# Kernel optimization log

Measured on AMD Instinct MI355X. Metric: run time of the kernel, lower is better.

## Reference

```python
import jax, jax.numpy as jnp
import numpy as np

TOKENS, D_IN, D_OUT, RANK = 32768, 1024, 1024, 16
SCALE1 = 8.0 / RANK   # alpha=8, rank=16
SCALE2 = 16.0 / RANK  # alpha=16, rank=16


def setup_inputs() -> dict:
    key = jax.random.key(0)
    ks = jax.random.split(key, 7)
    inv = 1.0 / np.sqrt(D_IN)
    return {
        "x": jax.random.normal(ks[0], (TOKENS, D_IN), jnp.float32),
        "W": jax.random.normal(ks[1], (D_OUT, D_IN), jnp.float32) * inv,
        "b": jax.random.normal(ks[2], (D_OUT,), jnp.float32) * 0.01,
        "A1": jax.random.normal(ks[3], (RANK, D_IN), jnp.float32) * inv,
        "B1": jax.random.normal(ks[4], (D_OUT, RANK), jnp.float32) * 0.01,
        "A2": jax.random.normal(ks[5], (RANK, D_IN), jnp.float32) * inv,
        "B2": jax.random.normal(ks[6], (D_OUT, RANK), jnp.float32) * 0.01,
    }


def reference(x, W, b, A1, B1, A2, B2):
    # base linear: [T, D_in] @ [D_in, D_out] + b
    out = jnp.einsum("ti,oi->to", x, W) + b
    # LoRA adapter 1: scale * (x @ A1^T) @ B1^T   (dropout=Identity in eval)
    out = out + SCALE1 * jnp.einsum("tr,or->to", jnp.einsum("ti,ri->tr", x, A1), B1)
    # LoRA adapter 2
    out = out + SCALE2 * jnp.einsum("tr,or->to", jnp.einsum("ti,ri->tr", x, A2), B2)
    return out
```

## Files before the change

### kernel.cpp

```cpp
#include <hip/hip_runtime.h>

#define TOKENS 32768
#define DIN 1024
#define DOUT 1024
#define RANK 16
#define SCALE1 0.5f
#define SCALE2 1.0f

#define BM 128
#define BN 128
#define BK 32

typedef __bf16 bf16x8 __attribute__((ext_vector_type(8)));
typedef float f32x4 __attribute__((ext_vector_type(4)));

__device__ __forceinline__ void load_lds16(const void* gptr, void* lptr) {
    __builtin_amdgcn_global_load_lds(
        (__attribute__((address_space(1))) void*)gptr,
        (__attribute__((address_space(3))) void*)lptr, 16, 0, 0);
}

__global__ void weff_kernel(const float* __restrict__ W, const float* __restrict__ A1,
                            const float* __restrict__ B1, const float* __restrict__ A2,
                            const float* __restrict__ B2, __bf16* __restrict__ Weff) {
    int idx = blockIdx.x * blockDim.x + threadIdx.x;
    int o = idx >> 10;
    int i = idx & 1023;
    float s1 = 0.f, s2 = 0.f;
#pragma unroll
    for (int r = 0; r < RANK; ++r) {
        s1 += B1[o * RANK + r] * A1[r * DIN + i];
        s2 += B2[o * RANK + r] * A2[r * DIN + i];
    }
    Weff[idx] = (__bf16)(W[idx] + SCALE1 * s1 + SCALE2 * s2);
}

__global__ void cvt_x_kernel(const float* __restrict__ x, __bf16* __restrict__ xb) {
    int i = (blockIdx.x * blockDim.x + threadIdx.x) * 8;
    float4 a = *(const float4*)(x + i);
    float4 b = *(const float4*)(x + i + 4);
    bf16x8 v;
    v[0] = (__bf16)a.x; v[1] = (__bf16)a.y; v[2] = (__bf16)a.z; v[3] = (__bf16)a.w;
    v[4] = (__bf16)b.x; v[5] = (__bf16)b.y; v[6] = (__bf16)b.z; v[7] = (__bf16)b.w;
    *(bf16x8*)(xb + i) = v;
}

__global__ __launch_bounds__(256) void gemm_bt_kernel(
    const __bf16* __restrict__ A,
    const __bf16* __restrict__ Bw,
    const float* __restrict__ bias, float* __restrict__ C) {
    __shared__ __bf16 lsA[BM * BK];
    __shared__ __bf16 lsB[BN * BK];

    const int tid = threadIdx.x;
    const int wave = tid >> 6;
    const int lane = tid & 63;
    const int m0 = blockIdx.y * BM;
    const int n0 = blockIdx.x * BN;
    const int wm = wave >> 1;
    const int wn = wave & 1;

    const int lrow = lane >> 2;
    const int lcol = ((lane & 3) ^ ((lane >> 3) & 3)) * 8;

    const __bf16* gA = A + (size_t)(m0 + wave * 32 + lrow) * DIN + lcol;
    const __bf16* gB = Bw + (size_t)(n0 + wave * 32 + lrow) * DIN + lcol;
    __bf16* lA0 = &lsA[(wave * 32) * BK];
    __bf16* lA1 = &lsA[(wave * 32 + 16) * BK];
    __bf16* lB0 = &lsB[(wave * 32) * BK];
    __bf16* lB1 = &lsB[(wave * 32 + 16) * BK];

    f32x4 acc[4][4];
#pragma unroll
    for (int i = 0; i < 4; ++i)
#pragma unroll
        for (int j = 0; j < 4; ++j) acc[i][j] = f32x4{0.f, 0.f, 0.f, 0.f};

    const int fr = lane & 15;
    const int fsw = (((lane >> 4) ^ ((lane >> 1) & 3))) * 8;

    for (int k0 = 0; k0 < DIN; k0 += BK) {
        load_lds16(gA + k0, lA0);
        load_lds16(gA + k0 + 16 * DIN, lA1);
        load_lds16(gB + k0, lB0);
        load_lds16(gB + k0 + 16 * DIN, lB1);
        __syncthreads();

        bf16x8 af[4], bfv[4];
#pragma unroll
        for (int t = 0; t < 4; ++t) {
            af[t] = *(const bf16x8*)&lsA[(wm * 64 + t * 16 + fr) * BK + fsw];
            bfv[t] = *(const bf16x8*)&lsB[(wn * 64 + t * 16 + fr) * BK + fsw];
        }
#pragma unroll
        for (int mt = 0; mt < 4; ++mt)
#pragma unroll
            for (int nt = 0; nt < 4; ++nt)
                acc[mt][nt] = __builtin_amdgcn_mfma_f32_16x16x32_bf16(
                    af[mt], bfv[nt], acc[mt][nt], 0, 0, 0);
        __syncthreads();
    }

    const int rbase = (lane >> 4) * 4;
#pragma unroll
    for (int nt = 0; nt < 4; ++nt) {
        const int n = n0 + wn * 64 + nt * 16 + fr;
        const float bv = bias[n];
#pragma unroll
        for (int mt = 0; mt < 4; ++mt) {
            const int m = m0 + wm * 64 + mt * 16 + rbase;
            float* cp = C + (size_t)m * DOUT + n;
#pragma unroll
            for (int r = 0; r < 4; ++r) cp[(size_t)r * DOUT] = acc[mt][nt][r] + bv;
        }
    }
}

extern "C" void kernel_launch(void* const* d_in, const int* in_sizes, int n_in,
                              void* d_out, int out_size, void* d_ws, size_t ws_size,
                              hipStream_t stream) {
    const float* x  = (const float*)d_in[0];
    const float* W  = (const float*)d_in[1];
    const float* b  = (const float*)d_in[2];
    const float* A1 = (const float*)d_in[3];
    const float* B1 = (const float*)d_in[4];
    const float* A2 = (const float*)d_in[5];
    const float* B2 = (const float*)d_in[6];
    float* out = (float*)d_out;

    __bf16* xb   = (__bf16*)d_ws;
    __bf16* Weff = (__bf16*)((char*)d_ws + (size_t)TOKENS * DIN * sizeof(__bf16));

    cvt_x_kernel<<<TOKENS * DIN / (256 * 8), 256, 0, stream>>>(x, xb);
    weff_kernel<<<DOUT * DIN / 256, 256, 0, stream>>>(W, A1, B1, A2, B2, Weff);
    gemm_bt_kernel<<<dim3(DOUT / BN, TOKENS / BM), 256, 0, stream>>>(xb, Weff, b, out);
}
```

Measured before the change: 347.7 us.

## Double-buffer LDS tiles in GEMM to overlap global loads with MFMA

The GEMM kernel now keeps two LDS buffers for the A and B tiles. It prefetches the next K-tile with direct global-to-LDS loads while computing on the current one, which cuts the barriers per iteration from two to one. The aim is to hide global load latency behind the MFMA work. In exchange, LDS use per block doubles. The overlap may also be lost if the compiler inserts a conservative wait on the outstanding LDS-DMA loads before the fragment reads.

```diff
diff --git a/kernel.cpp b/kernel.cpp
--- a/kernel.cpp
+++ b/kernel.cpp
@@ -49,8 +49,8 @@
     const __bf16* __restrict__ A,
     const __bf16* __restrict__ Bw,
     const float* __restrict__ bias, float* __restrict__ C) {
-    __shared__ __bf16 lsA[BM * BK];
-    __shared__ __bf16 lsB[BN * BK];
+    __shared__ alignas(16) __bf16 lsA[2][BM * BK];
+    __shared__ alignas(16) __bf16 lsB[2][BN * BK];
 
     const int tid = threadIdx.x;
     const int wave = tid >> 6;
@@ -65,10 +65,8 @@
 
     const __bf16* gA = A + (size_t)(m0 + wave * 32 + lrow) * DIN + lcol;
     const __bf16* gB = Bw + (size_t)(n0 + wave * 32 + lrow) * DIN + lcol;
-    __bf16* lA0 = &lsA[(wave * 32) * BK];
-    __bf16* lA1 = &lsA[(wave * 32 + 16) * BK];
-    __bf16* lB0 = &lsB[(wave * 32) * BK];
-    __bf16* lB1 = &lsB[(wave * 32 + 16) * BK];
+    const int so0 = (wave * 32) * BK;
+    const int so1 = (wave * 32 + 16) * BK;
 
     f32x4 acc[4][4];
 #pragma unroll
@@ -77,20 +75,30 @@
         for (int j = 0; j < 4; ++j) acc[i][j] = f32x4{0.f, 0.f, 0.f, 0.f};
 
     const int fr = lane & 15;
-    const int fsw = (((lane >> 4) ^ ((lane >> 1) & 3))) * 8;
+    const int fsw = ((lane >> 4) ^ ((lane >> 1) & 3)) * 8;
 
+    load_lds16(gA, &lsA[0][so0]);
+    load_lds16(gA + 16 * DIN, &lsA[0][so1]);
+    load_lds16(gB, &lsB[0][so0]);
+    load_lds16(gB + 16 * DIN, &lsB[0][so1]);
+
+    int cur = 0;
     for (int k0 = 0; k0 < DIN; k0 += BK) {
-        load_lds16(gA + k0, lA0);
-        load_lds16(gA + k0 + 16 * DIN, lA1);
-        load_lds16(gB + k0, lB0);
-        load_lds16(gB + k0 + 16 * DIN, lB1);
         __syncthreads();
+
+        if (k0 + BK < DIN) {
+            const int kn = k0 + BK;
+            load_lds16(gA + kn, &lsA[cur ^ 1][so0]);
+            load_lds16(gA + kn + 16 * DIN, &lsA[cur ^ 1][so1]);
+            load_lds16(gB + kn, &lsB[cur ^ 1][so0]);
+            load_lds16(gB + kn + 16 * DIN, &lsB[cur ^ 1][so1]);
+        }
 
         bf16x8 af[4], bfv[4];
 #pragma unroll
         for (int t = 0; t < 4; ++t) {
-            af[t] = *(const bf16x8*)&lsA[(wm * 64 + t * 16 + fr) * BK + fsw];
-            bfv[t] = *(const bf16x8*)&lsB[(wn * 64 + t * 16 + fr) * BK + fsw];
+            af[t] = *(const bf16x8*)&lsA[cur][(wm * 64 + t * 16 + fr) * BK + fsw];
+            bfv[t] = *(const bf16x8*)&lsB[cur][(wn * 64 + t * 16 + fr) * BK + fsw];
         }
 #pragma unroll
         for (int mt = 0; mt < 4; ++mt)
@@ -98,7 +106,7 @@
             for (int nt = 0; nt < 4; ++nt)
                 acc[mt][nt] = __builtin_amdgcn_mfma_f32_16x16x32_bf16(
                     af[mt], bfv[nt], acc[mt][nt], 0, 0, 0);
-        __syncthreads();
+        cur ^= 1;
     }
 
     const int rbase = (lane >> 4) * 4;
```

Result: no change. 341.6 us (-1.7%).
